# Kernel optimization log

Measured on AMD Instinct MI355X. Metric: run time of the kernel, lower is better.

## Reference

```python
import jax, jax.numpy as jnp
import numpy as np


def setup_inputs() -> dict:
    key = jax.random.key(0)
    k1, k2, k3, k4 = jax.random.split(key, 4)
    n = 1000000
    nnz = 18000000
    ncols = 8
    field = jax.random.normal(k1, (n, ncols), dtype=jnp.float32)
    lap_vals = jax.random.normal(k2, (nnz,), dtype=jnp.float32)
    lap_row = jax.random.randint(k3, (nnz,), 0, n, dtype=jnp.int32).astype(jnp.int64)
    lap_col = jax.random.randint(k4, (nnz,), 0, n, dtype=jnp.int32).astype(jnp.int64)
    return {"field": field, "lap_vals": lap_vals, "lap_row": lap_row,
            "lap_col": lap_col, "n_vertices": n}


def reference(field, lap_vals, lap_row, lap_col, n_vertices):
    """Apply sparse Laplacian (COO, duplicates summed) to all field columns at once.

    Equivalent to torch.sparse.mm(L, field) where L = coo(row, col, vals, (n, n)).
    One fused gather-multiply-scatter pass replaces the per-column loop.
    """
    field = field.astype(jnp.float32)
    # gather: [nnz, ncols]
    contrib = lap_vals[:, None] * field[lap_col]
    # scatter-add over rows: [n, ncols]
    out = jax.ops.segment_sum(contrib, lap_row, num_segments=n_vertices)
    return out
```

## Files before the change

kernel.cpp:

```cpp
#include <hip/hip_runtime.h>

#define NCOLS 8
#define BLOCK 256
#define NB    512
#define NBKT  1024
#define RPB   1024

__device__ __forceinline__ int detect_is64(const void* p, int* s_flag) {
    if (threadIdx.x == 0) {
        const unsigned* w = (const unsigned*)p;
        int is64 = 1;
        #pragma unroll
        for (int k = 0; k < 16; ++k) is64 &= (w[2 * k + 1] == 0u) ? 1 : 0;
        *s_flag = is64;
    }
    __syncthreads();
    return *s_flag;
}

__device__ __forceinline__ int load_idx(const void* p, int i, int is64) {
    return is64 ? (int)((const long long*)p)[i] : ((const int*)p)[i];
}

__global__ __launch_bounds__(BLOCK) void k_zero_counts(unsigned* __restrict__ counts) {
    int i = blockIdx.x * BLOCK + threadIdx.x;
    if (i < NBKT) counts[i] = 0u;
}

__global__ __launch_bounds__(BLOCK) void k_hist(
    const void* __restrict__ rowp, int nnz, int chunk,
    unsigned* __restrict__ counts, unsigned* __restrict__ blockhist)
{
    __shared__ unsigned h[NBKT];
    __shared__ int s_flag;
    const int is64 = detect_is64(rowp, &s_flag);
    for (int b = threadIdx.x; b < NBKT; b += BLOCK) h[b] = 0u;
    __syncthreads();

    const int beg = blockIdx.x * chunk;
    const int end = min(nnz, beg + chunk);
    for (int i = beg + threadIdx.x; i < end; i += BLOCK) {
        int r = load_idx(rowp, i, is64);
        atomicAdd(&h[r >> 10], 1u);
    }
    __syncthreads();
    for (int b = threadIdx.x; b < NBKT; b += BLOCK) {
        unsigned c = h[b];
        blockhist[(size_t)blockIdx.x * NBKT + b] = c;
        if (c) atomicAdd(&counts[b], c);
    }
}

__global__ __launch_bounds__(NBKT) void k_scan(
    const unsigned* __restrict__ counts,
    unsigned* __restrict__ base, unsigned* __restrict__ cursor)
{
    __shared__ unsigned s[NBKT];
    const int t = threadIdx.x;
    const unsigned c = counts[t];
    s[t] = c;
    __syncthreads();
    for (int off = 1; off < NBKT; off <<= 1) {
        unsigned v = (t >= off) ? s[t - off] : 0u;
        __syncthreads();
        s[t] += v;
        __syncthreads();
    }
    const unsigned excl = s[t] - c;
    base[t] = excl;
    cursor[t] = excl;
    if (t == NBKT - 1) base[NBKT] = s[t];
}

__global__ __launch_bounds__(BLOCK) void k_scatter(
    const float* __restrict__ vals, const void* __restrict__ rowp,
    const void* __restrict__ colp, int nnz, int chunk,
    const unsigned* __restrict__ blockhist, unsigned* __restrict__ cursor,
    uint2* __restrict__ records)
{
    __shared__ unsigned lcur[NBKT];
    __shared__ int s_flag;
    const int is64 = detect_is64(rowp, &s_flag);

    for (int b = threadIdx.x; b < NBKT; b += BLOCK) {
        unsigned h = blockhist[(size_t)blockIdx.x * NBKT + b];
        lcur[b] = h ? atomicAdd(&cursor[b], h) : 0u;
    }
    __syncthreads();

    const int beg = blockIdx.x * chunk;
    const int end = min(nnz, beg + chunk);
    for (int i = beg + threadIdx.x; i < end; i += BLOCK) {
        int r = load_idx(rowp, i, is64);
        int c = load_idx(colp, i, is64);
        float v = vals[i];
        unsigned pos = atomicAdd(&lcur[r >> 10], 1u);
        records[pos] = make_uint2(((unsigned)(r & (RPB - 1)) << 20) | (unsigned)c,
                                  __float_as_uint(v));
    }
}

__global__ __launch_bounds__(BLOCK) void k_accum(
    const uint2* __restrict__ records, const unsigned* __restrict__ base,
    const float* __restrict__ field, float* __restrict__ out, int n)
{
    __shared__ float acc[NCOLS * RPB];
    for (int i = threadIdx.x; i < NCOLS * RPB; i += BLOCK) acc[i] = 0.f;
    __syncthreads();

    const int b = blockIdx.x;
    const unsigned beg = base[b], end = base[b + 1];
    for (unsigned i = beg + threadIdx.x; i < end; i += BLOCK) {
        uint2 rec = records[i];
        unsigned col = rec.x & 0xFFFFFu;
        unsigned lr  = rec.x >> 20;
        float v = __uint_as_float(rec.y);
        const float4* f = (const float4*)(field + (size_t)col * NCOLS);
        float4 f0 = f[0];
        float4 f1 = f[1];
        atomicAdd(&acc[0 * RPB + lr], v * f0.x);
        atomicAdd(&acc[1 * RPB + lr], v * f0.y);
        atomicAdd(&acc[2 * RPB + lr], v * f0.z);
        atomicAdd(&acc[3 * RPB + lr], v * f0.w);
        atomicAdd(&acc[4 * RPB + lr], v * f1.x);
        atomicAdd(&acc[5 * RPB + lr], v * f1.y);
        atomicAdd(&acc[6 * RPB + lr], v * f1.z);
        atomicAdd(&acc[7 * RPB + lr], v * f1.w);
    }
    __syncthreads();

    const size_t row0 = (size_t)b * RPB;
    for (int t = threadIdx.x; t < NCOLS * RPB; t += BLOCK) {
        int r = t >> 3, j = t & 7;
        size_t gr = row0 + (size_t)r;
        if (gr < (size_t)n) out[gr * NCOLS + j] = acc[j * RPB + r];
    }
}

__global__ __launch_bounds__(BLOCK) void lap_zero_kernel(float4* __restrict__ out, int n4) {
    int i = blockIdx.x * BLOCK + threadIdx.x;
    if (i < n4) out[i] = make_float4(0.f, 0.f, 0.f, 0.f);
}

__global__ __launch_bounds__(BLOCK) void lap_spmm_atomic(
    const float* __restrict__ vals, const void* __restrict__ rowp,
    const void* __restrict__ colp, const float* __restrict__ field,
    float* __restrict__ out, int nnz)
{
    __shared__ int s_flag;
    const int is64 = detect_is64(rowp, &s_flag);
    int i = blockIdx.x * BLOCK + threadIdx.x;
    if (i >= nnz) return;
    float v = vals[i];
    int r = load_idx(rowp, i, is64);
    int c = load_idx(colp, i, is64);
    const float4* f = (const float4*)(field + (size_t)c * NCOLS);
    float4 f0 = f[0], f1 = f[1];
    float* o = out + (size_t)r * NCOLS;
    unsafeAtomicAdd(o + 0, v * f0.x);
    unsafeAtomicAdd(o + 1, v * f0.y);
    unsafeAtomicAdd(o + 2, v * f0.z);
    unsafeAtomicAdd(o + 3, v * f0.w);
    unsafeAtomicAdd(o + 4, v * f1.x);
    unsafeAtomicAdd(o + 5, v * f1.y);
    unsafeAtomicAdd(o + 6, v * f1.z);
    unsafeAtomicAdd(o + 7, v * f1.w);
}

extern "C" void kernel_launch(void* const* d_in, const int* in_sizes, int n_in,
                              void* d_out, int out_size, void* d_ws, size_t ws_size,
                              hipStream_t stream) {
    const float* field = (const float*)d_in[0];
    const float* vals  = (const float*)d_in[1];
    const void*  rowp  = d_in[2];
    const void*  colp  = d_in[3];
    float* out = (float*)d_out;

    const int nnz = in_sizes[1];
    const int n   = out_size / NCOLS;

    const size_t off_counts    = 0;
    const size_t off_base      = 8192;
    const size_t off_cursor    = 16384;
    const size_t off_blockhist = 24576;
    const size_t off_records   = off_blockhist + (size_t)NB * NBKT * 4;
    const size_t need = off_records + (size_t)nnz * 8;

    if (ws_size < need || n > NBKT * RPB) {
        const int n4 = out_size / 4;
        lap_zero_kernel<<<(n4 + BLOCK - 1) / BLOCK, BLOCK, 0, stream>>>((float4*)out, n4);
        lap_spmm_atomic<<<(nnz + BLOCK - 1) / BLOCK, BLOCK, 0, stream>>>(
            vals, rowp, colp, field, out, nnz);
        return;
    }

    char* ws = (char*)d_ws;
    unsigned* counts    = (unsigned*)(ws + off_counts);
    unsigned* base      = (unsigned*)(ws + off_base);
    unsigned* cursor    = (unsigned*)(ws + off_cursor);
    unsigned* blockhist = (unsigned*)(ws + off_blockhist);
    uint2*    records   = (uint2*)   (ws + off_records);

    const int chunk = (nnz + NB - 1) / NB;

    k_zero_counts<<<(NBKT + BLOCK - 1) / BLOCK, BLOCK, 0, stream>>>(counts);
    k_hist<<<NB, BLOCK, 0, stream>>>(rowp, nnz, chunk, counts, blockhist);
    k_scan<<<1, NBKT, 0, stream>>>(counts, base, cursor);
    k_scatter<<<NB, BLOCK, 0, stream>>>(vals, rowp, colp, nnz, chunk,
                                        blockhist, cursor, records);
    k_accum<<<NBKT, BLOCK, 0, stream>>>(records, base, field, out, n);
}
```

Before: 1.283 ms.

## Use 2048 smaller row buckets, pad global counters, and vectorize record loads

Templates the binned COO SpMM on bucket count and switches the default to 2048 buckets of 512 rows, so each accumulation block needs half the shared memory and more blocks can stay resident (launch bounds now request 6 waves). Global bucket counters and cursors are padded to 16 words apart to cut atomic contention on shared cache lines. Bucket sizes are rounded up to multiples of four so the accumulation loop can read four records with two 16-byte loads and keep four field gathers in flight at once. The cost is a larger workspace, a longer scan, and slightly more unused record slots.

```diff
diff --git a/kernel.cpp b/kernel.cpp
--- a/kernel.cpp
+++ b/kernel.cpp
@@ -3,8 +3,7 @@
 #define NCOLS 8
 #define BLOCK 256
 #define NB    512
-#define NBKT  1024
-#define RPB   1024
+#define CPAD  16
 
 __device__ __forceinline__ int detect_is64(const void* p, int* s_flag) {
     if (threadIdx.x == 0) {
@@ -22,11 +21,12 @@
     return is64 ? (int)((const long long*)p)[i] : ((const int*)p)[i];
 }
 
-__global__ __launch_bounds__(BLOCK) void k_zero_counts(unsigned* __restrict__ counts) {
+__global__ __launch_bounds__(BLOCK) void k_zero_counts(unsigned* __restrict__ counts, int nwords) {
     int i = blockIdx.x * BLOCK + threadIdx.x;
-    if (i < NBKT) counts[i] = 0u;
-}
-
+    if (i < nwords) counts[i] = 0u;
+}
+
+template<int NBKT, int LG2RPB>
 __global__ __launch_bounds__(BLOCK) void k_hist(
     const void* __restrict__ rowp, int nnz, int chunk,
     unsigned* __restrict__ counts, unsigned* __restrict__ blockhist)
@@ -41,37 +41,50 @@
     const int end = min(nnz, beg + chunk);
     for (int i = beg + threadIdx.x; i < end; i += BLOCK) {
         int r = load_idx(rowp, i, is64);
-        atomicAdd(&h[r >> 10], 1u);
+        atomicAdd(&h[r >> LG2RPB], 1u);
     }
     __syncthreads();
     for (int b = threadIdx.x; b < NBKT; b += BLOCK) {
         unsigned c = h[b];
         blockhist[(size_t)blockIdx.x * NBKT + b] = c;
-        if (c) atomicAdd(&counts[b], c);
-    }
-}
-
-__global__ __launch_bounds__(NBKT) void k_scan(
+        if (c) atomicAdd(&counts[(size_t)b * CPAD], c);
+    }
+}
+
+template<int NBKT>
+__global__ __launch_bounds__(1024) void k_scan(
     const unsigned* __restrict__ counts,
     unsigned* __restrict__ base, unsigned* __restrict__ cursor)
 {
-    __shared__ unsigned s[NBKT];
+    __shared__ unsigned s[1024];
     const int t = threadIdx.x;
-    const unsigned c = counts[t];
-    s[t] = c;
-    __syncthreads();
-    for (int off = 1; off < NBKT; off <<= 1) {
+    constexpr int E = NBKT / 1024;
+    unsigned c[E];
+    unsigned sum = 0;
+    #pragma unroll
+    for (int e = 0; e < E; ++e) {
+        c[e] = (counts[(size_t)(t * E + e) * CPAD] + 3u) & ~3u;
+        sum += c[e];
+    }
+    s[t] = sum;
+    __syncthreads();
+    for (int off = 1; off < 1024; off <<= 1) {
         unsigned v = (t >= off) ? s[t - off] : 0u;
         __syncthreads();
         s[t] += v;
         __syncthreads();
     }
-    const unsigned excl = s[t] - c;
-    base[t] = excl;
-    cursor[t] = excl;
-    if (t == NBKT - 1) base[NBKT] = s[t];
-}
-
+    unsigned excl = s[t] - sum;
+    #pragma unroll
+    for (int e = 0; e < E; ++e) {
+        base[t * E + e] = excl;
+        cursor[(size_t)(t * E + e) * CPAD] = excl;
+        excl += c[e];
+    }
+    if (t == 1023) base[NBKT] = s[t];
+}
+
+template<int NBKT, int LG2RPB>
 __global__ __launch_bounds__(BLOCK) void k_scatter(
     const float* __restrict__ vals, const void* __restrict__ rowp,
     const void* __restrict__ colp, int nnz, int chunk,
@@ -84,24 +97,27 @@
 
     for (int b = threadIdx.x; b < NBKT; b += BLOCK) {
         unsigned h = blockhist[(size_t)blockIdx.x * NBKT + b];
-        lcur[b] = h ? atomicAdd(&cursor[b], h) : 0u;
+        lcur[b] = h ? atomicAdd(&cursor[(size_t)b * CPAD], h) : 0u;
     }
     __syncthreads();
 
     const int beg = blockIdx.x * chunk;
     const int end = min(nnz, beg + chunk);
+    constexpr unsigned RM = (1u << LG2RPB) - 1u;
     for (int i = beg + threadIdx.x; i < end; i += BLOCK) {
         int r = load_idx(rowp, i, is64);
         int c = load_idx(colp, i, is64);
         float v = vals[i];
-        unsigned pos = atomicAdd(&lcur[r >> 10], 1u);
-        records[pos] = make_uint2(((unsigned)(r & (RPB - 1)) << 20) | (unsigned)c,
+        unsigned pos = atomicAdd(&lcur[r >> LG2RPB], 1u);
+        records[pos] = make_uint2((((unsigned)r & RM) << 20) | (unsigned)c,
                                   __float_as_uint(v));
     }
 }
 
-__global__ __launch_bounds__(BLOCK) void k_accum(
+template<int RPB>
+__global__ __launch_bounds__(BLOCK, 6) void k_accum(
     const uint2* __restrict__ records, const unsigned* __restrict__ base,
+    const unsigned* __restrict__ cursor,
     const float* __restrict__ field, float* __restrict__ out, int n)
 {
     __shared__ float acc[NCOLS * RPB];
@@ -109,23 +125,88 @@
     __syncthreads();
 
     const int b = blockIdx.x;
-    const unsigned beg = base[b], end = base[b + 1];
-    for (unsigned i = beg + threadIdx.x; i < end; i += BLOCK) {
-        uint2 rec = records[i];
-        unsigned col = rec.x & 0xFFFFFu;
-        unsigned lr  = rec.x >> 20;
-        float v = __uint_as_float(rec.y);
-        const float4* f = (const float4*)(field + (size_t)col * NCOLS);
-        float4 f0 = f[0];
-        float4 f1 = f[1];
-        atomicAdd(&acc[0 * RPB + lr], v * f0.x);
-        atomicAdd(&acc[1 * RPB + lr], v * f0.y);
-        atomicAdd(&acc[2 * RPB + lr], v * f0.z);
-        atomicAdd(&acc[3 * RPB + lr], v * f0.w);
-        atomicAdd(&acc[4 * RPB + lr], v * f1.x);
-        atomicAdd(&acc[5 * RPB + lr], v * f1.y);
-        atomicAdd(&acc[6 * RPB + lr], v * f1.z);
-        atomicAdd(&acc[7 * RPB + lr], v * f1.w);
+    const unsigned beg = base[b];
+    const unsigned end = cursor[(size_t)b * CPAD];
+    const unsigned cnt = end - beg;
+    const unsigned nq  = cnt >> 2;
+
+    for (unsigned q = threadIdx.x; q < nq; q += BLOCK) {
+        const unsigned i = beg + (q << 2);
+        const uint4 ra = *(const uint4*)(records + i);
+        const uint4 rb = *(const uint4*)(records + i + 2);
+
+        const unsigned k0 = ra.x, k1 = ra.z, k2 = rb.x, k3 = rb.z;
+        const float v0 = __uint_as_float(ra.y);
+        const float v1 = __uint_as_float(ra.w);
+        const float v2 = __uint_as_float(rb.y);
+        const float v3 = __uint_as_float(rb.w);
+
+        const float4* p0 = (const float4*)(field + (size_t)(k0 & 0xFFFFFu) * NCOLS);
+        const float4* p1 = (const float4*)(field + (size_t)(k1 & 0xFFFFFu) * NCOLS);
+        const float4* p2 = (const float4*)(field + (size_t)(k2 & 0xFFFFFu) * NCOLS);
+        const float4* p3 = (const float4*)(field + (size_t)(k3 & 0xFFFFFu) * NCOLS);
+        const float4 a0 = p0[0], b0 = p0[1];
+        const float4 a1 = p1[0], b1 = p1[1];
+        const float4 a2 = p2[0], b2 = p2[1];
+        const float4 a3 = p3[0], b3 = p3[1];
+
+        const unsigned l0 = k0 >> 20, l1 = k1 >> 20, l2 = k2 >> 20, l3 = k3 >> 20;
+
+        atomicAdd(&acc[0 * RPB + l0], v0 * a0.x);
+        atomicAdd(&acc[1 * RPB + l0], v0 * a0.y);
+        atomicAdd(&acc[2 * RPB + l0], v0 * a0.z);
+        atomicAdd(&acc[3 * RPB + l0], v0 * a0.w);
+        atomicAdd(&acc[4 * RPB + l0], v0 * b0.x);
+        atomicAdd(&acc[5 * RPB + l0], v0 * b0.y);
+        atomicAdd(&acc[6 * RPB + l0], v0 * b0.z);
+        atomicAdd(&acc[7 * RPB + l0], v0 * b0.w);
+
+        atomicAdd(&acc[0 * RPB + l1], v1 * a1.x);
+        atomicAdd(&acc[1 * RPB + l1], v1 * a1.y);
+        atomicAdd(&acc[2 * RPB + l1], v1 * a1.z);
+        atomicAdd(&acc[3 * RPB + l1], v1 * a1.w);
+        atomicAdd(&acc[4 * RPB + l1], v1 * b1.x);
+        atomicAdd(&acc[5 * RPB + l1], v1 * b1.y);
+        atomicAdd(&acc[6 * RPB + l1], v1 * b1.z);
+        atomicAdd(&acc[7 * RPB + l1], v1 * b1.w);
+
+        atomicAdd(&acc[0 * RPB + l2], v2 * a2.x);
+        atomicAdd(&acc[1 * RPB + l2], v2 * a2.y);
+        atomicAdd(&acc[2 * RPB + l2], v2 * a2.z);
+        atomicAdd(&acc[3 * RPB + l2], v2 * a2.w);
+        atomicAdd(&acc[4 * RPB + l2], v2 * b2.x);
+        atomicAdd(&acc[5 * RPB + l2], v2 * b2.y);
+        atomicAdd(&acc[6 * RPB + l2], v2 * b2.z);
+        atomicAdd(&acc[7 * RPB + l2], v2 * b2.w);
+
+        atomicAdd(&acc[0 * RPB + l3], v3 * a3.x);
+        atomicAdd(&acc[1 * RPB + l3], v3 * a3.y);
+        atomicAdd(&acc[2 * RPB + l3], v3 * a3.z);
+        atomicAdd(&acc[3 * RPB + l3], v3 * a3.w);
+        atomicAdd(&acc[4 * RPB + l3], v3 * b3.x);
+        atomicAdd(&acc[5 * RPB + l3], v3 * b3.y);
+        atomicAdd(&acc[6 * RPB + l3], v3 * b3.z);
+        atomicAdd(&acc[7 * RPB + l3], v3 * b3.w);
+    }
+
+    {
+        const unsigned i = beg + (nq << 2) + threadIdx.x;
+        if (i < end) {
+            const uint2 rec = records[i];
+            const unsigned col = rec.x & 0xFFFFFu;
+            const unsigned lr  = rec.x >> 20;
+            const float v = __uint_as_float(rec.y);
+            const float4* f = (const float4*)(field + (size_t)col * NCOLS);
+            const float4 f0 = f[0], f1 = f[1];
+            atomicAdd(&acc[0 * RPB + lr], v * f0.x);
+            atomicAdd(&acc[1 * RPB + lr], v * f0.y);
+            atomicAdd(&acc[2 * RPB + lr], v * f0.z);
+            atomicAdd(&acc[3 * RPB + lr], v * f0.w);
+            atomicAdd(&acc[4 * RPB + lr], v * f1.x);
+            atomicAdd(&acc[5 * RPB + lr], v * f1.y);
+            atomicAdd(&acc[6 * RPB + lr], v * f1.z);
+            atomicAdd(&acc[7 * RPB + lr], v * f1.w);
+        }
     }
     __syncthreads();
 
@@ -167,6 +248,45 @@
     unsafeAtomicAdd(o + 7, v * f1.w);
 }
 
+template<int NBKT, int LG2RPB>
+static void run_binned(const float* field, const float* vals, const void* rowp,
+                       const void* colp, float* out, int nnz, int n,
+                       char* ws, hipStream_t stream)
+{
+    constexpr int RPB = 1 << LG2RPB;
+    const size_t o_counts = 0;
+    const size_t o_base   = o_counts + (size_t)NBKT * CPAD * 4;
+    const size_t o_cursor = (o_base + (size_t)(NBKT + 1) * 4 + 255) & ~(size_t)255;
+    const size_t o_bh     = o_cursor + (size_t)NBKT * CPAD * 4;
+    const size_t o_rec    = o_bh + (size_t)NB * NBKT * 4;
+
+    unsigned* counts    = (unsigned*)(ws + o_counts);
+    unsigned* base      = (unsigned*)(ws + o_base);
+    unsigned* cursor    = (unsigned*)(ws + o_cursor);
+    unsigned* blockhist = (unsigned*)(ws + o_bh);
+    uint2*    records   = (uint2*)   (ws + o_rec);
+
+    const int chunk = (nnz + NB - 1) / NB;
+    const int nwords = NBKT * CPAD;
+
+    k_zero_counts<<<(nwords + BLOCK - 1) / BLOCK, BLOCK, 0, stream>>>(counts, nwords);
+    k_hist<NBKT, LG2RPB><<<NB, BLOCK, 0, stream>>>(rowp, nnz, chunk, counts, blockhist);
+    k_scan<NBKT><<<1, 1024, 0, stream>>>(counts, base, cursor);
+    k_scatter<NBKT, LG2RPB><<<NB, BLOCK, 0, stream>>>(vals, rowp, colp, nnz, chunk,
+                                                      blockhist, cursor, records);
+    k_accum<RPB><<<NBKT, BLOCK, 0, stream>>>(records, base, cursor, field, out, n);
+}
+
+template<int NBKT>
+static size_t ws_need(int nnz)
+{
+    const size_t o_base   = (size_t)NBKT * CPAD * 4;
+    const size_t o_cursor = (o_base + (size_t)(NBKT + 1) * 4 + 255) & ~(size_t)255;
+    const size_t o_bh     = o_cursor + (size_t)NBKT * CPAD * 4;
+    const size_t o_rec    = o_bh + (size_t)NB * NBKT * 4;
+    return o_rec + ((size_t)nnz + 4 * NBKT) * 8;
+}
+
 extern "C" void kernel_launch(void* const* d_in, const int* in_sizes, int n_in,
                               void* d_out, int out_size, void* d_ws, size_t ws_size,
                               hipStream_t stream) {
@@ -178,35 +298,19 @@
 
     const int nnz = in_sizes[1];
     const int n   = out_size / NCOLS;
-
-    const size_t off_counts    = 0;
-    const size_t off_base      = 8192;
-    const size_t off_cursor    = 16384;
-    const size_t off_blockhist = 24576;
-    const size_t off_records   = off_blockhist + (size_t)NB * NBKT * 4;
-    const size_t need = off_records + (size_t)nnz * 8;
-
-    if (ws_size < need || n > NBKT * RPB) {
-        const int n4 = out_size / 4;
-        lap_zero_kernel<<<(n4 + BLOCK - 1) / BLOCK, BLOCK, 0, stream>>>((float4*)out, n4);
-        lap_spmm_atomic<<<(nnz + BLOCK - 1) / BLOCK, BLOCK, 0, stream>>>(
-            vals, rowp, colp, field, out, nnz);
+    char* ws = (char*)d_ws;
+
+    if (ws_size >= ws_need<2048>(nnz) && n <= 2048 * 512) {
+        run_binned<2048, 9>(field, vals, rowp, colp, out, nnz, n, ws, stream);
         return;
     }
-
-    char* ws = (char*)d_ws;
-    unsigned* counts    = (unsigned*)(ws + off_counts);
-    unsigned* base      = (unsigned*)(ws + off_base);
-    unsigned* cursor    = (unsigned*)(ws + off_cursor);
-    unsigned* blockhist = (unsigned*)(ws + off_blockhist);
-    uint2*    records   = (uint2*)   (ws + off_records);
-
-    const int chunk = (nnz + NB - 1) / NB;
-
-    k_zero_counts<<<(NBKT + BLOCK - 1) / BLOCK, BLOCK, 0, stream>>>(counts);
-    k_hist<<<NB, BLOCK, 0, stream>>>(rowp, nnz, chunk, counts, blockhist);
-    k_scan<<<1, NBKT, 0, stream>>>(counts, base, cursor);
-    k_scatter<<<NB, BLOCK, 0, stream>>>(vals, rowp, colp, nnz, chunk,
-                                        blockhist, cursor, records);
-    k_accum<<<NBKT, BLOCK, 0, stream>>>(records, base, field, out, n);
-}
+    if (ws_size >= ws_need<1024>(nnz) && n <= 1024 * 1024) {
+        run_binned<1024, 10>(field, vals, rowp, colp, out, nnz, n, ws, stream);
+        return;
+    }
+
+    const int n4 = out_size / 4;
+    lap_zero_kernel<<<(n4 + BLOCK - 1) / BLOCK, BLOCK, 0, stream>>>((float4*)out, n4);
+    lap_spmm_atomic<<<(nnz + BLOCK - 1) / BLOCK, BLOCK, 0, stream>>>(
+        vals, rowp, colp, field, out, nnz);
+}
```

After: 1.413 ms. 10.1% more time.

## Sub-bucket records by column range in accumulation for field gather locality

Applied to the files above, without the earlier changes.

In the accumulation kernel, each row bucket's records are now regrouped by column range into a second scratch buffer, so field gathers within a block walk the columns in order. The hist/scatter stages become deterministic: a per-column prefix sum over block histograms replaces the global cursor atomics and the zero-counts launch, and the block count is halved. The extra pass reads and writes every record again, trading global traffic for better cache locality on the random field gather. It needs a second nnz-sized workspace and falls back to the old accumulation if that space is missing.

```diff
diff --git a/kernel.cpp b/kernel.cpp
--- a/kernel.cpp
+++ b/kernel.cpp
@@ -1,63 +1,61 @@
 #include <hip/hip_runtime.h>
 
-#define NCOLS 8
-#define BLOCK 256
-#define NB    512
-#define NBKT  1024
-#define RPB   1024
-
-__device__ __forceinline__ int detect_is64(const void* p, int* s_flag) {
-    if (threadIdx.x == 0) {
-        const unsigned* w = (const unsigned*)p;
-        int is64 = 1;
-        #pragma unroll
-        for (int k = 0; k < 16; ++k) is64 &= (w[2 * k + 1] == 0u) ? 1 : 0;
-        *s_flag = is64;
-    }
-    __syncthreads();
-    return *s_flag;
+#define NCOLS  8
+#define BLOCK  256
+#define NB     256
+#define NBKT   1024
+#define LG2RPB 10
+#define RPB    1024
+#define NCB    32
+
+__device__ __forceinline__ int detect_is64(const void* p) {
+    const unsigned* w = (const unsigned*)p;
+    int is64 = 1;
+    #pragma unroll
+    for (int k = 0; k < 16; ++k) is64 &= (w[2 * k + 1] == 0u) ? 1 : 0;
+    return is64;
 }
 
 __device__ __forceinline__ int load_idx(const void* p, int i, int is64) {
     return is64 ? (int)((const long long*)p)[i] : ((const int*)p)[i];
 }
 
-__global__ __launch_bounds__(BLOCK) void k_zero_counts(unsigned* __restrict__ counts) {
-    int i = blockIdx.x * BLOCK + threadIdx.x;
-    if (i < NBKT) counts[i] = 0u;
-}
-
 __global__ __launch_bounds__(BLOCK) void k_hist(
-    const void* __restrict__ rowp, int nnz, int chunk,
-    unsigned* __restrict__ counts, unsigned* __restrict__ blockhist)
+    const void* __restrict__ rowp, int nnz, int chunk, unsigned* __restrict__ hist)
 {
     __shared__ unsigned h[NBKT];
-    __shared__ int s_flag;
-    const int is64 = detect_is64(rowp, &s_flag);
-    for (int b = threadIdx.x; b < NBKT; b += BLOCK) h[b] = 0u;
-    __syncthreads();
-
+    const int is64 = detect_is64(rowp);
+    for (int i = threadIdx.x; i < NBKT; i += BLOCK) h[i] = 0u;
+    __syncthreads();
     const int beg = blockIdx.x * chunk;
     const int end = min(nnz, beg + chunk);
-    for (int i = beg + threadIdx.x; i < end; i += BLOCK) {
-        int r = load_idx(rowp, i, is64);
-        atomicAdd(&h[r >> 10], 1u);
-    }
-    __syncthreads();
-    for (int b = threadIdx.x; b < NBKT; b += BLOCK) {
-        unsigned c = h[b];
-        blockhist[(size_t)blockIdx.x * NBKT + b] = c;
-        if (c) atomicAdd(&counts[b], c);
-    }
-}
-
-__global__ __launch_bounds__(NBKT) void k_scan(
-    const unsigned* __restrict__ counts,
-    unsigned* __restrict__ base, unsigned* __restrict__ cursor)
+    for (int i = beg + threadIdx.x; i < end; i += BLOCK)
+        atomicAdd(&h[load_idx(rowp, i, is64) >> LG2RPB], 1u);
+    __syncthreads();
+    unsigned* row = hist + (size_t)blockIdx.x * NBKT;
+    for (int i = threadIdx.x; i < NBKT; i += BLOCK) row[i] = h[i];
+}
+
+__global__ __launch_bounds__(BLOCK) void k_colsum(
+    unsigned* __restrict__ hist, unsigned* __restrict__ total)
+{
+    const int c = blockIdx.x * BLOCK + threadIdx.x;
+    if (c >= NBKT) return;
+    unsigned run = 0;
+    for (int b = 0; b < NB; ++b) {
+        unsigned t = hist[(size_t)b * NBKT + c];
+        hist[(size_t)b * NBKT + c] = run;
+        run += t;
+    }
+    total[c] = run;
+}
+
+__global__ __launch_bounds__(1024) void k_scan(
+    const unsigned* __restrict__ total, unsigned* __restrict__ base)
 {
     __shared__ unsigned s[NBKT];
     const int t = threadIdx.x;
-    const unsigned c = counts[t];
+    const unsigned c = total[t];
     s[t] = c;
     __syncthreads();
     for (int off = 1; off < NBKT; off <<= 1) {
@@ -66,58 +64,117 @@
         s[t] += v;
         __syncthreads();
     }
-    const unsigned excl = s[t] - c;
-    base[t] = excl;
-    cursor[t] = excl;
+    base[t] = s[t] - c;
     if (t == NBKT - 1) base[NBKT] = s[t];
 }
 
 __global__ __launch_bounds__(BLOCK) void k_scatter(
     const float* __restrict__ vals, const void* __restrict__ rowp,
     const void* __restrict__ colp, int nnz, int chunk,
-    const unsigned* __restrict__ blockhist, unsigned* __restrict__ cursor,
+    const unsigned* __restrict__ hist, const unsigned* __restrict__ base,
     uint2* __restrict__ records)
 {
-    __shared__ unsigned lcur[NBKT];
-    __shared__ int s_flag;
-    const int is64 = detect_is64(rowp, &s_flag);
-
-    for (int b = threadIdx.x; b < NBKT; b += BLOCK) {
-        unsigned h = blockhist[(size_t)blockIdx.x * NBKT + b];
-        lcur[b] = h ? atomicAdd(&cursor[b], h) : 0u;
-    }
-    __syncthreads();
-
+    __shared__ unsigned cur[NBKT];
+    const int is64 = detect_is64(rowp);
+    const unsigned* pref = hist + (size_t)blockIdx.x * NBKT;
+    for (int i = threadIdx.x; i < NBKT; i += BLOCK) cur[i] = base[i] + pref[i];
+    __syncthreads();
     const int beg = blockIdx.x * chunk;
     const int end = min(nnz, beg + chunk);
     for (int i = beg + threadIdx.x; i < end; i += BLOCK) {
         int r = load_idx(rowp, i, is64);
         int c = load_idx(colp, i, is64);
         float v = vals[i];
-        unsigned pos = atomicAdd(&lcur[r >> 10], 1u);
-        records[pos] = make_uint2(((unsigned)(r & (RPB - 1)) << 20) | (unsigned)c,
+        unsigned pos = atomicAdd(&cur[r >> LG2RPB], 1u);
+        records[pos] = make_uint2((((unsigned)r & (RPB - 1u)) << 20) | (unsigned)c,
                                   __float_as_uint(v));
     }
 }
 
-__global__ __launch_bounds__(BLOCK) void k_accum(
+__global__ __launch_bounds__(BLOCK) void k_accum2(
+    const uint2* __restrict__ records, const unsigned* __restrict__ base,
+    uint2* __restrict__ scratch2, const float* __restrict__ field,
+    float* __restrict__ out, int n, int lg2cpb)
+{
+    __shared__ float acc[NCOLS * RPB];
+    __shared__ unsigned cnt[NCB];
+    __shared__ unsigned pref[NCB + 1];
+    __shared__ unsigned cur[NCB];
+
+    const int b = blockIdx.x;
+    const unsigned beg = base[b], end = base[b + 1];
+
+    for (int i = threadIdx.x; i < NCOLS * RPB; i += BLOCK) acc[i] = 0.f;
+    if (threadIdx.x < NCB) cnt[threadIdx.x] = 0u;
+    __syncthreads();
+
+    for (unsigned i = beg + threadIdx.x; i < end; i += BLOCK) {
+        unsigned cb = (records[i].x & 0xFFFFFu) >> lg2cpb;
+        atomicAdd(&cnt[cb], 1u);
+    }
+    __syncthreads();
+    if (threadIdx.x == 0) {
+        unsigned run = beg;
+        #pragma unroll
+        for (int k = 0; k < NCB; ++k) { pref[k] = run; cur[k] = run; run += cnt[k]; }
+        pref[NCB] = run;
+    }
+    __syncthreads();
+
+    for (unsigned i = beg + threadIdx.x; i < end; i += BLOCK) {
+        uint2 rec = records[i];
+        unsigned cb = (rec.x & 0xFFFFFu) >> lg2cpb;
+        unsigned pos = atomicAdd(&cur[cb], 1u);
+        scratch2[pos] = rec;
+    }
+    __threadfence_block();
+    __syncthreads();
+
+    for (int k = 0; k < NCB; ++k) {
+        const unsigned s0 = pref[k], s1 = pref[k + 1];
+        for (unsigned i = s0 + threadIdx.x; i < s1; i += BLOCK) {
+            const uint2 rec = scratch2[i];
+            const unsigned col = rec.x & 0xFFFFFu;
+            const unsigned lr  = rec.x >> 20;
+            const float v = __uint_as_float(rec.y);
+            const float4* f = (const float4*)(field + (size_t)col * NCOLS);
+            const float4 f0 = f[0], f1 = f[1];
+            atomicAdd(&acc[0 * RPB + lr], v * f0.x);
+            atomicAdd(&acc[1 * RPB + lr], v * f0.y);
+            atomicAdd(&acc[2 * RPB + lr], v * f0.z);
+            atomicAdd(&acc[3 * RPB + lr], v * f0.w);
+            atomicAdd(&acc[4 * RPB + lr], v * f1.x);
+            atomicAdd(&acc[5 * RPB + lr], v * f1.y);
+            atomicAdd(&acc[6 * RPB + lr], v * f1.z);
+            atomicAdd(&acc[7 * RPB + lr], v * f1.w);
+        }
+    }
+    __syncthreads();
+
+    const size_t row0 = (size_t)b * RPB;
+    for (int t = threadIdx.x; t < NCOLS * RPB; t += BLOCK) {
+        int r = t >> 3, j = t & 7;
+        size_t gr = row0 + (size_t)r;
+        if (gr < (size_t)n) out[gr * NCOLS + j] = acc[j * RPB + r];
+    }
+}
+
+__global__ __launch_bounds__(BLOCK) void k_accum1(
     const uint2* __restrict__ records, const unsigned* __restrict__ base,
     const float* __restrict__ field, float* __restrict__ out, int n)
 {
     __shared__ float acc[NCOLS * RPB];
     for (int i = threadIdx.x; i < NCOLS * RPB; i += BLOCK) acc[i] = 0.f;
     __syncthreads();
-
     const int b = blockIdx.x;
     const unsigned beg = base[b], end = base[b + 1];
     for (unsigned i = beg + threadIdx.x; i < end; i += BLOCK) {
-        uint2 rec = records[i];
-        unsigned col = rec.x & 0xFFFFFu;
-        unsigned lr  = rec.x >> 20;
-        float v = __uint_as_float(rec.y);
+        const uint2 rec = records[i];
+        const unsigned col = rec.x & 0xFFFFFu;
+        const unsigned lr  = rec.x >> 20;
+        const float v = __uint_as_float(rec.y);
         const float4* f = (const float4*)(field + (size_t)col * NCOLS);
-        float4 f0 = f[0];
-        float4 f1 = f[1];
+        const float4 f0 = f[0], f1 = f[1];
         atomicAdd(&acc[0 * RPB + lr], v * f0.x);
         atomicAdd(&acc[1 * RPB + lr], v * f0.y);
         atomicAdd(&acc[2 * RPB + lr], v * f0.z);
@@ -128,7 +185,6 @@
         atomicAdd(&acc[7 * RPB + lr], v * f1.w);
     }
     __syncthreads();
-
     const size_t row0 = (size_t)b * RPB;
     for (int t = threadIdx.x; t < NCOLS * RPB; t += BLOCK) {
         int r = t >> 3, j = t & 7;
@@ -147,8 +203,7 @@
     const void* __restrict__ colp, const float* __restrict__ field,
     float* __restrict__ out, int nnz)
 {
-    __shared__ int s_flag;
-    const int is64 = detect_is64(rowp, &s_flag);
+    const int is64 = detect_is64(rowp);
     int i = blockIdx.x * BLOCK + threadIdx.x;
     if (i >= nnz) return;
     float v = vals[i];
@@ -178,35 +233,43 @@
 
     const int nnz = in_sizes[1];
     const int n   = out_size / NCOLS;
-
-    const size_t off_counts    = 0;
-    const size_t off_base      = 8192;
-    const size_t off_cursor    = 16384;
-    const size_t off_blockhist = 24576;
-    const size_t off_records   = off_blockhist + (size_t)NB * NBKT * 4;
-    const size_t need = off_records + (size_t)nnz * 8;
-
-    if (ws_size < need || n > NBKT * RPB) {
-        const int n4 = out_size / 4;
-        lap_zero_kernel<<<(n4 + BLOCK - 1) / BLOCK, BLOCK, 0, stream>>>((float4*)out, n4);
-        lap_spmm_atomic<<<(nnz + BLOCK - 1) / BLOCK, BLOCK, 0, stream>>>(
-            vals, rowp, colp, field, out, nnz);
+    char* ws = (char*)d_ws;
+
+    const size_t o_hist  = 0;
+    const size_t o_total = o_hist + (size_t)NB * NBKT * 4;
+    const size_t o_base  = o_total + (size_t)NBKT * 4;
+    const size_t o_rec   = (o_base + (size_t)(NBKT + 1) * 4 + 255) & ~(size_t)255;
+    const size_t o_scr2  = o_rec + (size_t)nnz * 8;
+    const size_t need1   = o_scr2 + (size_t)nnz * 8;
+    const size_t need2   = o_scr2;
+
+    if (n <= NBKT * RPB && n <= (1 << 20) && ws_size >= need2) {
+        unsigned* hist  = (unsigned*)(ws + o_hist);
+        unsigned* total = (unsigned*)(ws + o_total);
+        unsigned* base  = (unsigned*)(ws + o_base);
+        uint2*    rec   = (uint2*)(ws + o_rec);
+        uint2*    scr2  = (uint2*)(ws + o_scr2);
+
+        const int chunk = (nnz + NB - 1) / NB;
+
+        k_hist<<<NB, BLOCK, 0, stream>>>(rowp, nnz, chunk, hist);
+        k_colsum<<<(NBKT + BLOCK - 1) / BLOCK, BLOCK, 0, stream>>>(hist, total);
+        k_scan<<<1, NBKT, 0, stream>>>(total, base);
+        k_scatter<<<NB, BLOCK, 0, stream>>>(vals, rowp, colp, nnz, chunk, hist, base, rec);
+
+        if (ws_size >= need1) {
+            int lg = 0;
+            while ((1u << lg) < (unsigned)n) ++lg;
+            int lg2cpb = lg > 5 ? lg - 5 : 0;
+            k_accum2<<<NBKT, BLOCK, 0, stream>>>(rec, base, scr2, field, out, n, lg2cpb);
+        } else {
+            k_accum1<<<NBKT, BLOCK, 0, stream>>>(rec, base, field, out, n);
+        }
         return;
     }
 
-    char* ws = (char*)d_ws;
-    unsigned* counts    = (unsigned*)(ws + off_counts);
-    unsigned* base      = (unsigned*)(ws + off_base);
-    unsigned* cursor    = (unsigned*)(ws + off_cursor);
-    unsigned* blockhist = (unsigned*)(ws + off_blockhist);
-    uint2*    records   = (uint2*)   (ws + off_records);
-
-    const int chunk = (nnz + NB - 1) / NB;
-
-    k_zero_counts<<<(NBKT + BLOCK - 1) / BLOCK, BLOCK, 0, stream>>>(counts);
-    k_hist<<<NB, BLOCK, 0, stream>>>(rowp, nnz, chunk, counts, blockhist);
-    k_scan<<<1, NBKT, 0, stream>>>(counts, base, cursor);
-    k_scatter<<<NB, BLOCK, 0, stream>>>(vals, rowp, colp, nnz, chunk,
-                                        blockhist, cursor, records);
-    k_accum<<<NBKT, BLOCK, 0, stream>>>(records, base, field, out, n);
-}
+    const int n4 = out_size / 4;
+    lap_zero_kernel<<<(n4 + BLOCK - 1) / BLOCK, BLOCK, 0, stream>>>((float4*)out, n4);
+    lap_spmm_atomic<<<(nnz + BLOCK - 1) / BLOCK, BLOCK, 0, stream>>>(
+        vals, rowp, colp, field, out, nnz);
+}
```

Result: slower. 1.374 ms (+7.0%).
